# Kernel tuning notes

Hardware: AMD Instinct MI355X
Metric: run time of the kernel (lower is better)

## Reference

```python
import jax, jax.numpy as jnp
import numpy as np

D1 = 512
D2 = 1024  # = 2*D1 (concat of x1,y1 along channels)
B, S = 4, 2048


def _self_attn(x, Wq, bq, Wk, bk, Wv, bv):
    # Linear layers use torch convention: out = x @ W.T + b
    q = jnp.einsum('bsd,ed->bse', x, Wq) + bq
    k = jnp.einsum('bsd,ed->bse', x, Wk) + bk
    v = jnp.einsum('bsd,ed->bse', x, Wv) + bv
    # NOTE: original module has no 1/sqrt(d) scaling — keep it faithful.
    scores = jnp.einsum('bqe,bke->bqk', q, k)  # [B,S,S]
    attn = jax.nn.softmax(scores, axis=-1)
    return jnp.einsum('bqk,bke->bqe', attn, v)


def setup_inputs() -> dict:
    key = jax.random.key(0)
    ks = jax.random.split(key, 18)
    s1 = 1.0 / np.sqrt(D1)
    s2 = 1.0 / np.sqrt(D2)
    return {
        'x': jax.random.normal(ks[0], (B, S, D1), jnp.float32),
        'y': jax.random.normal(ks[1], (B, S, D1), jnp.float32),
        'sa1_Wq': jax.random.normal(ks[2], (D1, D1), jnp.float32) * s1,
        'sa1_bq': jnp.zeros((D1,), jnp.float32),
        'sa1_Wk': jax.random.normal(ks[3], (D1, D1), jnp.float32) * s1,
        'sa1_bk': jnp.zeros((D1,), jnp.float32),
        'sa1_Wv': jax.random.normal(ks[4], (D1, D1), jnp.float32) * s1,
        'sa1_bv': jnp.zeros((D1,), jnp.float32),
        'sa2_Wq': jax.random.normal(ks[5], (D2, D2), jnp.float32) * s2,
        'sa2_bq': jnp.zeros((D2,), jnp.float32),
        'sa2_Wk': jax.random.normal(ks[6], (D2, D2), jnp.float32) * s2,
        'sa2_bk': jnp.zeros((D2,), jnp.float32),
        'sa2_Wv': jax.random.normal(ks[7], (D2, D2), jnp.float32) * s2,
        'sa2_bv': jnp.zeros((D2,), jnp.float32),
        'weight1': jnp.ones((1,), jnp.float32),
        'weight2': jnp.ones((1,), jnp.float32),
    }


def reference(x, y, sa1_Wq, sa1_bq, sa1_Wk, sa1_bk, sa1_Wv, sa1_bv,
              sa2_Wq, sa2_bq, sa2_Wk, sa2_bk, sa2_Wv, sa2_bv,
              weight1, weight2):
    x1 = _self_attn(x, sa1_Wq, sa1_bq, sa1_Wk, sa1_bk, sa1_Wv, sa1_bv)
    x1 = x1 + y * weight2
    y1 = _self_attn(y, sa1_Wq, sa1_bq, sa1_Wk, sa1_bk, sa1_Wv, sa1_bv)
    y1 = y1 + x * weight1
    temp = jnp.concatenate((x1, y1), axis=2)  # [B,S,2*D1]
    return _self_attn(temp, sa2_Wq, sa2_bq, sa2_Wk, sa2_bk, sa2_Wv, sa2_bv)
```

## Files before the change

### kernel.cpp

```cpp
#include <hip/hip_runtime.h>
#include <hip/hip_bf16.h>
#include <cstdint>
#include <cstddef>


typedef __bf16 bf16;
typedef __attribute__((ext_vector_type(8))) __bf16 bf16x8;
typedef __attribute__((ext_vector_type(4))) __bf16 bf16x4;
typedef __attribute__((ext_vector_type(4))) float f32x4;

__device__ __forceinline__ void gld16(const bf16* g, bf16* s) {
    __builtin_amdgcn_global_load_lds(
        (const __attribute__((address_space(1))) void*)g,
        (__attribute__((address_space(3))) void*)s, 16, 0, 0);
}

#define WAIT_VM8   __builtin_amdgcn_s_waitcnt(8 | (7 << 4) | (0xF << 8))
#define WAIT_VM0   __builtin_amdgcn_s_waitcnt(0 | (7 << 4) | (0xF << 8))
#define WAIT_LGKM0 __builtin_amdgcn_s_waitcnt(0xF | (7 << 4) | (0 << 8) | (3 << 14))

__device__ __forceinline__ int swz(int row, int g) {
    return row * 64 + ((g ^ (row & 7)) << 3);
}

__global__ __launch_bounds__(256) void gemm_split(
    const bf16* __restrict__ A, long lda, long psA, long bsA,
    const bf16* __restrict__ B, long ldb, long psB, long bsB,
    void* __restrict__ C, long ldc, long psC, long bsC, int mode,
    const float* __restrict__ bias,
    const float* __restrict__ resid, long ldr, long bsR,
    const float* __restrict__ scale,
    int K, int split, int nx, int ny)
{
    __shared__ __align__(16) bf16 As[2][128 * 64];
    __shared__ __align__(16) bf16 Bs[2][128 * 64];

    const int t    = threadIdx.x;
    const int wave = t >> 6;
    const int lane = t & 63;
    const int wr   = wave >> 1;
    const int wc   = wave & 1;
    const int r16  = lane & 15;
    const int quad = lane >> 4;

    const int g    = blockIdx.x;
    const int xcd  = g & 7;
    const int tk   = g >> 3;
    const int nst8 = gridDim.x >> 7;
    const int st   = xcd * nst8 + (tk >> 4);
    const int p    = tk & 15;
    const int snx  = nx >> 2, sny = ny >> 2;
    const int spz  = snx * sny;
    const int zz   = st / spz;
    const int rS   = st - zz * spz;
    const int sy   = rS / snx;
    const int sx   = rS - sy * snx;
    const int yb   = sy * 4 + (p >> 2);
    const int xb   = sx * 4 + (p & 3);
    const long z   = zz;

    const long row0 = (long)yb * 128;
    const long col0 = (long)xb * 128;

    const int srow = (lane >> 3);
    const int scol = ((lane & 7) ^ srow) * 8;

    const int ktiles = K >> 6;
    const int T = split * ktiles;

    const bf16* Az = A + z * bsA;
    const bf16* Bz = B + z * bsB;

    auto prefetch = [&](int ti, int buf) {
        const int ph = ti / ktiles;
        const int kt = (ti - ph * ktiles) << 6;
        const bf16* Ab = Az + (ph == 1 ? psA : 0);
        const bf16* Bb = Bz + (ph == 2 ? psB : 0);
#pragma unroll
        for (int p2 = 0; p2 < 4; ++p2) {
            const int chunk = wave * 32 + p2 * 8;
            gld16(Ab + (row0 + chunk + srow) * lda + kt + scol, &As[buf][chunk * 64]);
            gld16(Bb + (col0 + chunk + srow) * ldb + kt + scol, &Bs[buf][chunk * 64]);
        }
    };

    f32x4 acc[4][4];
#pragma unroll
    for (int r = 0; r < 4; ++r)
#pragma unroll
        for (int c = 0; c < 4; ++c)
            acc[r][c] = (f32x4){0.f, 0.f, 0.f, 0.f};

    prefetch(0, 0);
    prefetch(1, 1);
    for (int ti = 0; ti < T; ++ti) {
        const int cur = ti & 1;
        if (ti + 1 < T) WAIT_VM8; else WAIT_VM0;
        __builtin_amdgcn_s_barrier();
        bf16x8 af[2][4], bg[2][4];
#pragma unroll
        for (int kk = 0; kk < 2; ++kk) {
            const int g0 = (kk << 2) + quad;
#pragma unroll
            for (int r = 0; r < 4; ++r)
                af[kk][r] = *reinterpret_cast<const bf16x8*>(&As[cur][swz(wr * 64 + r * 16 + r16, g0)]);
#pragma unroll
            for (int c = 0; c < 4; ++c)
                bg[kk][c] = *reinterpret_cast<const bf16x8*>(&Bs[cur][swz(wc * 64 + c * 16 + r16, g0)]);
        }
        WAIT_LGKM0;
        __builtin_amdgcn_s_barrier();
        if (ti + 2 < T) prefetch(ti + 2, cur);
#pragma unroll
        for (int kk = 0; kk < 2; ++kk)
#pragma unroll
            for (int r = 0; r < 4; ++r)
#pragma unroll
                for (int c = 0; c < 4; ++c)
                    acc[r][c] = __builtin_amdgcn_mfma_f32_16x16x32_bf16(af[kk][r], bg[kk][c], acc[r][c], 0, 0, 0);
    }

    const float scv = resid ? *scale : 0.f;

#pragma unroll
    for (int r = 0; r < 4; ++r) {
#pragma unroll
        for (int c = 0; c < 4; ++c) {
            long gcol = col0 + wc * 64 + c * 16 + r16;
            float bv = bias ? bias[gcol] : 0.f;
#pragma unroll
            for (int i = 0; i < 4; ++i) {
                long grow = row0 + wr * 64 + r * 16 + quad * 4 + i;
                float val = acc[r][c][i] + bv;
                if (mode == 0) {
                    if (resid) val += resid[z * bsR + grow * ldr + gcol] * scv;
                    ((float*)C)[z * bsC + grow * ldc + gcol] = val;
                } else if (mode == 1) {
                    if (resid) val += resid[z * bsR + grow * ldr + gcol] * scv;
                    bf16* Cb = (bf16*)C + z * bsC;
                    bf16 h = (bf16)val;
                    Cb[grow * ldc + gcol] = h;
                    Cb[psC + grow * ldc + gcol] = (bf16)(val - (float)h);
                } else {
                    long b = grow >> 11, s = grow & 2047;
                    bf16* Cb = (bf16*)C + b * bsC;
                    bf16 h = (bf16)val;
                    Cb[gcol * ldc + s] = h;
                    Cb[psC + gcol * ldc + s] = (bf16)(val - (float)h);
                }
            }
        }
    }
}

__global__ __launch_bounds__(512) void gemm256_scores(
    const bf16* __restrict__ A, long lda, long psA, long bsA,
    const bf16* __restrict__ B, long ldb, long psB, long bsB,
    float* __restrict__ C, long ldc, long bsC, int K)
{
    __shared__ __align__(16) bf16 As[2][256 * 64];
    __shared__ __align__(16) bf16 Bs[2][256 * 64];

    const int t    = threadIdx.x;
    const int wave = t >> 6;
    const int lane = t & 63;
    const int wm   = wave >> 2;
    const int wn   = wave & 3;
    const int r16  = lane & 15;
    const int quad = lane >> 4;

    const int g   = blockIdx.x;
    const int idx = (g & 7) * 32 + (g >> 3);
    const int z   = idx >> 6;
    const int t6  = idx & 63;
    const int ty  = t6 >> 3;
    const int tx  = t6 & 7;
    const long row0 = (long)ty * 256;
    const long col0 = (long)tx * 256;

    const int srow = lane >> 3;
    const int scol = ((lane & 7) ^ srow) * 8;

    const int ktiles = K >> 6;
    const int T = 3 * ktiles;

    const bf16* Az = A + (long)z * bsA;
    const bf16* Bz = B + (long)z * bsB;

    auto prefetch = [&](int ti, int buf) {
        const int ph = ti / ktiles;
        const int kt = (ti - ph * ktiles) << 6;
        const bf16* Ab = Az + (ph == 1 ? psA : 0);
        const bf16* Bb = Bz + (ph == 2 ? psB : 0);
#pragma unroll
        for (int p2 = 0; p2 < 4; ++p2) {
            const int chunk = wave * 32 + p2 * 8;
            gld16(Ab + (row0 + chunk + srow) * lda + kt + scol, &As[buf][chunk * 64]);
            gld16(Bb + (col0 + chunk + srow) * ldb + kt + scol, &Bs[buf][chunk * 64]);
        }
    };

    f32x4 acc[8][4];
#pragma unroll
    for (int r = 0; r < 8; ++r)
#pragma unroll
        for (int c = 0; c < 4; ++c)
            acc[r][c] = (f32x4){0.f, 0.f, 0.f, 0.f};

    prefetch(0, 0);
    prefetch(1, 1);
    for (int ti = 0; ti < T; ++ti) {
        const int cur = ti & 1;
        if (ti + 1 < T) WAIT_VM8; else WAIT_VM0;
        __builtin_amdgcn_s_barrier();

        bf16x8 afA[4][2], afB[4][2], bg[2][2][2];
#pragma unroll
        for (int kk = 0; kk < 2; ++kk) {
            const int g0 = (kk << 2) + quad;
#pragma unroll
            for (int r = 0; r < 4; ++r)
                afA[r][kk] = *reinterpret_cast<const bf16x8*>(
                    &As[cur][swz(wm * 128 + r * 16 + r16, g0)]);
        }
#pragma unroll
        for (int kk = 0; kk < 2; ++kk) {
            const int g0 = (kk << 2) + quad;
#pragma unroll
            for (int c = 0; c < 2; ++c)
                bg[0][c][kk] = *reinterpret_cast<const bf16x8*>(
                    &Bs[cur][swz(wn * 64 + c * 16 + r16, g0)]);
        }
#pragma unroll
        for (int kk = 0; kk < 2; ++kk) {
            const int g0 = (kk << 2) + quad;
#pragma unroll
            for (int c = 0; c < 2; ++c)
                bg[1][c][kk] = *reinterpret_cast<const bf16x8*>(
                    &Bs[cur][swz(wn * 64 + (2 + c) * 16 + r16, g0)]);
        }
#pragma unroll
        for (int kk = 0; kk < 2; ++kk) {
            const int g0 = (kk << 2) + quad;
#pragma unroll
            for (int r = 0; r < 4; ++r)
                afB[r][kk] = *reinterpret_cast<const bf16x8*>(
                    &As[cur][swz(wm * 128 + (4 + r) * 16 + r16, g0)]);
        }

        __builtin_amdgcn_s_setprio(1);
#pragma unroll
        for (int kk = 0; kk < 2; ++kk)
#pragma unroll
            for (int r = 0; r < 4; ++r)
#pragma unroll
                for (int c = 0; c < 2; ++c)
                    acc[r][c] = __builtin_amdgcn_mfma_f32_16x16x32_bf16(
                        afA[r][kk], bg[0][c][kk], acc[r][c], 0, 0, 0);
#pragma unroll
        for (int kk = 0; kk < 2; ++kk)
#pragma unroll
            for (int r = 0; r < 4; ++r)
#pragma unroll
                for (int c = 0; c < 2; ++c)
                    acc[r][2 + c] = __builtin_amdgcn_mfma_f32_16x16x32_bf16(
                        afA[r][kk], bg[1][c][kk], acc[r][2 + c], 0, 0, 0);
        __builtin_amdgcn_s_setprio(0);

        __builtin_amdgcn_sched_barrier(0);
        WAIT_LGKM0;
        __builtin_amdgcn_s_barrier();
        if (ti + 2 < T) prefetch(ti + 2, cur);

        __builtin_amdgcn_s_setprio(1);
#pragma unroll
        for (int kk = 0; kk < 2; ++kk)
#pragma unroll
            for (int r = 0; r < 4; ++r)
#pragma unroll
                for (int c = 0; c < 2; ++c)
                    acc[4 + r][c] = __builtin_amdgcn_mfma_f32_16x16x32_bf16(
                        afB[r][kk], bg[0][c][kk], acc[4 + r][c], 0, 0, 0);
#pragma unroll
        for (int kk = 0; kk < 2; ++kk)
#pragma unroll
            for (int r = 0; r < 4; ++r)
#pragma unroll
                for (int c = 0; c < 2; ++c)
                    acc[4 + r][2 + c] = __builtin_amdgcn_mfma_f32_16x16x32_bf16(
                        afB[r][kk], bg[1][c][kk], acc[4 + r][2 + c], 0, 0, 0);
        __builtin_amdgcn_s_setprio(0);
    }

#pragma unroll
    for (int r = 0; r < 8; ++r) {
#pragma unroll
        for (int c = 0; c < 4; ++c) {
            const long gcol = col0 + wn * 64 + c * 16 + r16;
#pragma unroll
            for (int i = 0; i < 4; ++i) {
                const long grow = row0 + wm * 128 + r * 16 + quad * 4 + i;
                C[(long)z * bsC + grow * ldc + gcol] = acc[r][c][i];
            }
        }
    }
}

__global__ __launch_bounds__(256) void softmax_planes(float* __restrict__ S)
{
    __shared__ float redm[4], reds[4];
    float* srow = S + (long)blockIdx.x * 2048;
    const int t = threadIdx.x;
    const int lane = t & 63;
    const int wave = t >> 6;

    f32x4 v0 = *reinterpret_cast<const f32x4*>(srow + t * 4);
    f32x4 v1 = *reinterpret_cast<const f32x4*>(srow + 1024 + t * 4);

    float m = v0[0];
#pragma unroll
    for (int i = 1; i < 4; ++i) m = fmaxf(m, v0[i]);
#pragma unroll
    for (int i = 0; i < 4; ++i) m = fmaxf(m, v1[i]);
#pragma unroll
    for (int off = 32; off > 0; off >>= 1) m = fmaxf(m, __shfl_xor(m, off));
    if (lane == 0) redm[wave] = m;
    __syncthreads();
    m = fmaxf(fmaxf(redm[0], redm[1]), fmaxf(redm[2], redm[3]));

    float s = 0.f;
#pragma unroll
    for (int i = 0; i < 4; ++i) { v0[i] = __expf(v0[i] - m); s += v0[i]; }
#pragma unroll
    for (int i = 0; i < 4; ++i) { v1[i] = __expf(v1[i] - m); s += v1[i]; }
#pragma unroll
    for (int off = 32; off > 0; off >>= 1) s += __shfl_xor(s, off);
    if (lane == 0) reds[wave] = s;
    __syncthreads();
    s = reds[0] + reds[1] + reds[2] + reds[3];
    float inv = 1.f / s;

    bf16x4 h0, h1, l0, l1;
#pragma unroll
    for (int i = 0; i < 4; ++i) {
        float a = v0[i] * inv, b = v1[i] * inv;
        h0[i] = (bf16)a; l0[i] = (bf16)(a - (float)h0[i]);
        h1[i] = (bf16)b; l1[i] = (bf16)(b - (float)h1[i]);
    }
    bf16* ph = (bf16*)srow;
    *reinterpret_cast<bf16x4*>(ph + t * 4) = h0;
    *reinterpret_cast<bf16x4*>(ph + 1024 + t * 4) = h1;
    *reinterpret_cast<bf16x4*>(ph + 2048 + t * 4) = l0;
    *reinterpret_cast<bf16x4*>(ph + 3072 + t * 4) = l1;
}

__global__ __launch_bounds__(256) void split_f32(
    const float* __restrict__ in, bf16* __restrict__ hi, long n)
{
    long i = ((long)blockIdx.x * 256 + threadIdx.x) * 4;
    f32x4 v = *reinterpret_cast<const f32x4*>(in + i);
    bf16x4 h, l;
#pragma unroll
    for (int j = 0; j < 4; ++j) {
        h[j] = (bf16)v[j];
        l[j] = (bf16)(v[j] - (float)h[j]);
    }
    *reinterpret_cast<bf16x4*>(hi + i) = h;
    *reinterpret_cast<bf16x4*>(hi + n + i) = l;
}

extern "C" void kernel_launch(void* const* d_in, const int* in_sizes, int n_in,
                              void* d_out, int out_size, void* d_ws, size_t ws_size,
                              hipStream_t stream)
{
    const float* x   = (const float*)d_in[0];
    const float* y   = (const float*)d_in[1];
    const float* Wq1 = (const float*)d_in[2];
    const float* bq1 = (const float*)d_in[3];
    const float* Wk1 = (const float*)d_in[4];
    const float* bk1 = (const float*)d_in[5];
    const float* Wv1 = (const float*)d_in[6];
    const float* bv1 = (const float*)d_in[7];
    const float* Wq2 = (const float*)d_in[8];
    const float* bq2 = (const float*)d_in[9];
    const float* Wk2 = (const float*)d_in[10];
    const float* bk2 = (const float*)d_in[11];
    const float* Wv2 = (const float*)d_in[12];
    const float* bv2 = (const float*)d_in[13];
    const float* w1  = (const float*)d_in[14];
    const float* w2  = (const float*)d_in[15];
    float* out = (float*)d_out;

    const size_t MB = 1ull << 20;
    char* ws = (char*)d_ws;
    const long S = 2048, M4 = 8192, E1 = 512, E2 = 1024;
    const long W1ps = E1 * E1, W2ps = E2 * E2;

    const int cfg = (ws_size >= 207 * MB) ? 2 : 0;

    bf16 *Wq1p, *Wk1p, *Wv1p, *Wq2p, *Wk2p, *Wv2p, *temp, *qb, *kb, *vt;
    float* Sc;
    bf16* xp = (bf16*)d_out;
    bf16* yp = xp + 2 * M4 * E1;
    if (cfg == 2) {
        Wq1p = (bf16*)(ws + 0 * MB);  Wk1p = (bf16*)(ws + 1 * MB);  Wv1p = (bf16*)(ws + 2 * MB);
        Wq2p = (bf16*)(ws + 3 * MB);  Wk2p = (bf16*)(ws + 7 * MB);  Wv2p = (bf16*)(ws + 11 * MB);
        temp = (bf16*)(ws + 15 * MB);
        qb   = (bf16*)(ws + 47 * MB);
        kb   = (bf16*)(ws + 79 * MB);
        vt   = (bf16*)(ws + 111 * MB);
        Sc   = (float*)(ws + 143 * MB);
    } else {
        Wq1p = (bf16*)(ws + 0 * MB);  Wk1p = (bf16*)(ws + 1 * MB);  Wv1p = (bf16*)(ws + 2 * MB);
        temp = (bf16*)(ws + 3 * MB);
        qb   = (bf16*)(ws + 35 * MB);
        kb   = (bf16*)(ws + 43 * MB);
        vt   = (bf16*)(ws + 51 * MB);
        Sc   = (float*)(ws + 59 * MB);
        Wq2p = (bf16*)d_out;
        Wk2p = Wq2p + 2 * W2ps;
        Wv2p = Wk2p + 2 * W2ps;
    }

    auto gemm = [&](const bf16* A, long lda, long psA, long bsA,
                    const bf16* B, long ldb, long psB, long bsB,
                    void* C, long ldc, long psC, long bsC, int mode,
                    const float* bias, const float* resid, long ldr, long bsR,
                    const float* scale, int M, int N, int K, int split, int gz) {
        int nx = N / 128, ny = M / 128;
        dim3 g((unsigned)(nx * ny * gz));
        gemm_split<<<g, dim3(256), 0, stream>>>(
            A, lda, psA, bsA, B, ldb, psB, bsB, C, ldc, psC, bsC, mode,
            bias, resid, ldr, bsR, scale, K, split, nx, ny);
    };
    auto scores256 = [&](const bf16* A, long lda, long psA, long bsA,
                         const bf16* B, long ldb, long psB, long bsB,
                         float* C, int K) {
        gemm256_scores<<<dim3(256), dim3(512), 0, stream>>>(
            A, lda, psA, bsA, B, ldb, psB, bsB, C, S, S * S, K);
    };
    auto conv = [&](const float* in, bf16* planes, long n) {
        split_f32<<<dim3((unsigned)(n / 1024)), dim3(256), 0, stream>>>(in, planes, n);
    };

    conv(x, xp, M4 * E1);
    conv(y, yp, M4 * E1);
    conv(Wq1, Wq1p, W1ps); conv(Wk1, Wk1p, W1ps); conv(Wv1, Wv1p, W1ps);
    if (cfg == 2) { conv(Wq2, Wq2p, W2ps); conv(Wk2, Wk2p, W2ps); conv(Wv2, Wv2p, W2ps); }

    auto stage1 = [&](const bf16* sp, const float* resid, const float* scale, long colOff) {
        if (cfg == 2) {
            gemm(sp, E1, M4 * E1, 0, Wq1p, E1, W1ps, 0, qb, E1, M4 * E1, 0, 1,
                 bq1, nullptr, 0, 0, nullptr, 8192, 512, 512, 3, 1);
            gemm(sp, E1, M4 * E1, 0, Wk1p, E1, W1ps, 0, kb, E1, M4 * E1, 0, 1,
                 bk1, nullptr, 0, 0, nullptr, 8192, 512, 512, 3, 1);
            gemm(sp, E1, M4 * E1, 0, Wv1p, E1, W1ps, 0, vt, S, E1 * S, 2 * E1 * S, 2,
                 bv1, nullptr, 0, 0, nullptr, 8192, 512, 512, 3, 1);
            scores256(qb, E1, M4 * E1, S * E1, kb, E1, M4 * E1, S * E1, Sc, 512);
            softmax_planes<<<dim3(8192), dim3(256), 0, stream>>>(Sc);
            gemm((const bf16*)Sc, 4096, 2048, S * 4096, vt, S, E1 * S, 2 * E1 * S,
                 temp + colOff, 1024, M4 * 1024, S * 1024, 1,
                 nullptr, resid, E1, S * E1, scale, 2048, 512, 2048, 3, 4);
        } else {
            for (int b = 0; b < 4; ++b) {
                const bf16* sb = sp + (long)b * S * E1;
                gemm(sb, E1, M4 * E1, 0, Wq1p, E1, W1ps, 0, qb, E1, S * E1, 0, 1,
                     bq1, nullptr, 0, 0, nullptr, 2048, 512, 512, 3, 1);
                gemm(sb, E1, M4 * E1, 0, Wk1p, E1, W1ps, 0, kb, E1, S * E1, 0, 1,
                     bk1, nullptr, 0, 0, nullptr, 2048, 512, 512, 3, 1);
                gemm(sb, E1, M4 * E1, 0, Wv1p, E1, W1ps, 0, vt, S, E1 * S, 0, 2,
                     bv1, nullptr, 0, 0, nullptr, 2048, 512, 512, 3, 1);
                gemm(qb, E1, S * E1, 0, kb, E1, S * E1, 0, Sc, S, 0, 0, 0,
                     nullptr, nullptr, 0, 0, nullptr, 2048, 2048, 512, 3, 1);
                softmax_planes<<<dim3(2048), dim3(256), 0, stream>>>(Sc);
                gemm((const bf16*)Sc, 4096, 2048, 0, vt, S, E1 * S, 0,
                     temp + colOff + (long)b * S * 1024, 1024, M4 * 1024, 0, 1,
                     nullptr, resid + (long)b * S * E1, E1, 0, scale, 2048, 512, 2048, 3, 1);
            }
        }
    };

    stage1(xp, y, w2, 0);
    stage1(yp, x, w1, 512);

    if (cfg == 0) { conv(Wq2, Wq2p, W2ps); conv(Wk2, Wk2p, W2ps); conv(Wv2, Wv2p, W2ps); }

    if (cfg == 2) {
        gemm(temp, E2, M4 * E2, 0, Wq2p, E2, W2ps, 0, qb, E2, M4 * E2, 0, 1,
             bq2, nullptr, 0, 0, nullptr, 8192, 1024, 1024, 3, 1);
        gemm(temp, E2, M4 * E2, 0, Wk2p, E2, W2ps, 0, kb, E2, M4 * E2, 0, 1,
             bk2, nullptr, 0, 0, nullptr, 8192, 1024, 1024, 3, 1);
        gemm(temp, E2, M4 * E2, 0, Wv2p, E2, W2ps, 0, vt, S, E2 * S, 2 * E2 * S, 2,
             bv2, nullptr, 0, 0, nullptr, 8192, 1024, 1024, 1, 1);
        scores256(qb, E2, M4 * E2, S * E2, kb, E2, M4 * E2, S * E2, Sc, 1024);
        softmax_planes<<<dim3(8192), dim3(256), 0, stream>>>(Sc);
        gemm((const bf16*)Sc, 4096, 2048, S * 4096, vt, S, E2 * S, 2 * E2 * S,
             out, E2, 0, S * E2, 0, nullptr, nullptr, 0, 0, nullptr,
             2048, 1024, 2048, 1, 4);
    } else {
        for (int b = 0; b < 4; ++b) {
            const bf16* tb = temp + (long)b * S * E2;
            gemm(tb, E2, M4 * E2, 0, Wq2p, E2, W2ps, 0, qb, E2, S * E2, 0, 1,
                 bq2, nullptr, 0, 0, nullptr, 2048, 1024, 1024, 3, 1);
            gemm(tb, E2, M4 * E2, 0, Wk2p, E2, W2ps, 0, kb, E2, S * E2, 0, 1,
                 bk2, nullptr, 0, 0, nullptr, 2048, 1024, 1024, 3, 1);
            gemm(tb, E2, M4 * E2, 0, Wv2p, E2, W2ps, 0, vt, S, E2 * S, 0, 2,
                 bv2, nullptr, 0, 0, nullptr, 2048, 1024, 1024, 1, 1);
            gemm(qb, E2, S * E2, 0, kb, E2, S * E2, 0, Sc, S, 0, 0, 0,
                 nullptr, nullptr, 0, 0, nullptr, 2048, 2048, 1024, 3, 1);
            softmax_planes<<<dim3(2048), dim3(256), 0, stream>>>(Sc);
            gemm((const bf16*)Sc, 4096, 2048, 0, vt, S, E2 * S, 0,
                 out + (long)b * S * E2, E2, 0, 0, 0, nullptr, nullptr, 0, 0, nullptr,
                 2048, 1024, 2048, 1, 1);
        }
    }

    (void)in_sizes; (void)n_in; (void)out_size;
}
```

Measured before the change: 986.5 us.

## Fuse Q/K projections and batch x/y stage-1 projections into single GEMMs

For the large-workspace path, Wq and Wk are concatenated into one weight matrix so Q and K come from a single GEMM, with a split bias selected per column. The x and y inputs are packed contiguously so the stage-1 projections for both run as one GEMM with M=16384 instead of separate launches. This cuts kernel launches and rereads of the A operand, and gives each GEMM a larger grid. In exchange the weight and activation buffers need reorganized plane layouts, and the epilogue does a per-column branch to pick the bias.

```diff
diff --git a/kernel.cpp b/kernel.cpp
--- a/kernel.cpp
+++ b/kernel.cpp
@@ -27,7 +27,7 @@
     const bf16* __restrict__ A, long lda, long psA, long bsA,
     const bf16* __restrict__ B, long ldb, long psB, long bsB,
     void* __restrict__ C, long ldc, long psC, long bsC, int mode,
-    const float* __restrict__ bias,
+    const float* __restrict__ bias, const float* __restrict__ bias2, int nsplit,
     const float* __restrict__ resid, long ldr, long bsR,
     const float* __restrict__ scale,
     int K, int split, int nx, int ny)
@@ -127,7 +127,8 @@
 #pragma unroll
         for (int c = 0; c < 4; ++c) {
             long gcol = col0 + wc * 64 + c * 16 + r16;
-            float bv = bias ? bias[gcol] : 0.f;
+            float bv = 0.f;
+            if (bias) bv = (gcol < nsplit) ? bias[gcol] : bias2[gcol - nsplit];
 #pragma unroll
             for (int i = 0; i < 4; ++i) {
                 long grow = row0 + wr * 64 + r * 16 + quad * 4 + i;
@@ -354,8 +355,8 @@
     *reinterpret_cast<bf16x4*>(ph + 3072 + t * 4) = l1;
 }
 
-__global__ __launch_bounds__(256) void split_f32(
-    const float* __restrict__ in, bf16* __restrict__ hi, long n)
+__global__ __launch_bounds__(256) void split2_f32(
+    const float* __restrict__ in, bf16* __restrict__ hi, bf16* __restrict__ lo)
 {
     long i = ((long)blockIdx.x * 256 + threadIdx.x) * 4;
     f32x4 v = *reinterpret_cast<const f32x4*>(in + i);
@@ -366,7 +367,7 @@
         l[j] = (bf16)(v[j] - (float)h[j]);
     }
     *reinterpret_cast<bf16x4*>(hi + i) = h;
-    *reinterpret_cast<bf16x4*>(hi + n + i) = l;
+    *reinterpret_cast<bf16x4*>(lo + i) = l;
 }
 
 extern "C" void kernel_launch(void* const* d_in, const int* in_sizes, int n_in,
@@ -398,40 +399,17 @@
 
     const int cfg = (ws_size >= 207 * MB) ? 2 : 0;
 
-    bf16 *Wq1p, *Wk1p, *Wv1p, *Wq2p, *Wk2p, *Wv2p, *temp, *qb, *kb, *vt;
-    float* Sc;
-    bf16* xp = (bf16*)d_out;
-    bf16* yp = xp + 2 * M4 * E1;
-    if (cfg == 2) {
-        Wq1p = (bf16*)(ws + 0 * MB);  Wk1p = (bf16*)(ws + 1 * MB);  Wv1p = (bf16*)(ws + 2 * MB);
-        Wq2p = (bf16*)(ws + 3 * MB);  Wk2p = (bf16*)(ws + 7 * MB);  Wv2p = (bf16*)(ws + 11 * MB);
-        temp = (bf16*)(ws + 15 * MB);
-        qb   = (bf16*)(ws + 47 * MB);
-        kb   = (bf16*)(ws + 79 * MB);
-        vt   = (bf16*)(ws + 111 * MB);
-        Sc   = (float*)(ws + 143 * MB);
-    } else {
-        Wq1p = (bf16*)(ws + 0 * MB);  Wk1p = (bf16*)(ws + 1 * MB);  Wv1p = (bf16*)(ws + 2 * MB);
-        temp = (bf16*)(ws + 3 * MB);
-        qb   = (bf16*)(ws + 35 * MB);
-        kb   = (bf16*)(ws + 43 * MB);
-        vt   = (bf16*)(ws + 51 * MB);
-        Sc   = (float*)(ws + 59 * MB);
-        Wq2p = (bf16*)d_out;
-        Wk2p = Wq2p + 2 * W2ps;
-        Wv2p = Wk2p + 2 * W2ps;
-    }
-
     auto gemm = [&](const bf16* A, long lda, long psA, long bsA,
                     const bf16* B, long ldb, long psB, long bsB,
                     void* C, long ldc, long psC, long bsC, int mode,
-                    const float* bias, const float* resid, long ldr, long bsR,
+                    const float* bias, const float* bias2, int nsplit,
+                    const float* resid, long ldr, long bsR,
                     const float* scale, int M, int N, int K, int split, int gz) {
         int nx = N / 128, ny = M / 128;
         dim3 g((unsigned)(nx * ny * gz));
         gemm_split<<<g, dim3(256), 0, stream>>>(
             A, lda, psA, bsA, B, ldb, psB, bsB, C, ldc, psC, bsC, mode,
-            bias, resid, ldr, bsR, scale, K, split, nx, ny);
+            bias, bias2, nsplit, resid, ldr, bsR, scale, K, split, nx, ny);
     };
     auto scores256 = [&](const bf16* A, long lda, long psA, long bsA,
                          const bf16* B, long ldb, long psB, long bsB,
@@ -439,79 +417,131 @@
         gemm256_scores<<<dim3(256), dim3(512), 0, stream>>>(
             A, lda, psA, bsA, B, ldb, psB, bsB, C, S, S * S, K);
     };
-    auto conv = [&](const float* in, bf16* planes, long n) {
-        split_f32<<<dim3((unsigned)(n / 1024)), dim3(256), 0, stream>>>(in, planes, n);
+    auto conv2 = [&](const float* in, bf16* hi, bf16* lo, long n) {
+        split2_f32<<<dim3((unsigned)(n / 1024)), dim3(256), 0, stream>>>(in, hi, lo);
     };
 
-    conv(x, xp, M4 * E1);
-    conv(y, yp, M4 * E1);
-    conv(Wq1, Wq1p, W1ps); conv(Wk1, Wk1p, W1ps); conv(Wv1, Wv1p, W1ps);
-    if (cfg == 2) { conv(Wq2, Wq2p, W2ps); conv(Wk2, Wk2p, W2ps); conv(Wv2, Wv2p, W2ps); }
-
-    auto stage1 = [&](const bf16* sp, const float* resid, const float* scale, long colOff) {
-        if (cfg == 2) {
-            gemm(sp, E1, M4 * E1, 0, Wq1p, E1, W1ps, 0, qb, E1, M4 * E1, 0, 1,
-                 bq1, nullptr, 0, 0, nullptr, 8192, 512, 512, 3, 1);
-            gemm(sp, E1, M4 * E1, 0, Wk1p, E1, W1ps, 0, kb, E1, M4 * E1, 0, 1,
-                 bk1, nullptr, 0, 0, nullptr, 8192, 512, 512, 3, 1);
-            gemm(sp, E1, M4 * E1, 0, Wv1p, E1, W1ps, 0, vt, S, E1 * S, 2 * E1 * S, 2,
-                 bv1, nullptr, 0, 0, nullptr, 8192, 512, 512, 3, 1);
-            scores256(qb, E1, M4 * E1, S * E1, kb, E1, M4 * E1, S * E1, Sc, 512);
-            softmax_planes<<<dim3(8192), dim3(256), 0, stream>>>(Sc);
-            gemm((const bf16*)Sc, 4096, 2048, S * 4096, vt, S, E1 * S, 2 * E1 * S,
-                 temp + colOff, 1024, M4 * 1024, S * 1024, 1,
-                 nullptr, resid, E1, S * E1, scale, 2048, 512, 2048, 3, 4);
-        } else {
+    if (cfg == 2) {
+        bf16* xyp   = (bf16*)d_out;
+        bf16* Wqk1p = (bf16*)(ws + 0 * MB);
+        bf16* Wv1p  = (bf16*)(ws + 2 * MB);
+        bf16* Wqk2p = (bf16*)(ws + 3 * MB);
+        bf16* Wv2p  = (bf16*)(ws + 11 * MB);
+        bf16* temp  = (bf16*)(ws + 15 * MB);
+        bf16* qk    = (bf16*)(ws + 47 * MB);
+        bf16* vt    = (bf16*)(ws + 111 * MB);
+        float* Sc   = (float*)(ws + 143 * MB);
+
+        const long PXY = 16384L * 512;
+        const long PW1 = 1024L * 512;
+        const long PW2 = 2048L * 1024;
+        const long PQ1 = 16384L * 1024;
+        const long PQ2 = 8192L * 2048;
+        const long PT  = 8192L * 1024;
+        const long BV1 = 2 * E1 * S;
+        const long BV2 = 2 * E2 * S;
+
+        conv2(x, xyp, xyp + PXY, M4 * E1);
+        conv2(y, xyp + M4 * E1, xyp + PXY + M4 * E1, M4 * E1);
+        conv2(Wq1, Wqk1p, Wqk1p + PW1, W1ps);
+        conv2(Wk1, Wqk1p + W1ps, Wqk1p + PW1 + W1ps, W1ps);
+        conv2(Wv1, Wv1p, Wv1p + W1ps, W1ps);
+        conv2(Wq2, Wqk2p, Wqk2p + PW2, W2ps);
+        conv2(Wk2, Wqk2p + W2ps, Wqk2p + PW2 + W2ps, W2ps);
+        conv2(Wv2, Wv2p, Wv2p + W2ps, W2ps);
+
+        gemm(xyp, E1, PXY, 0, Wqk1p, E1, PW1, 0,
+             qk, 1024, PQ1, 0, 1, bq1, bk1, 512,
+             nullptr, 0, 0, nullptr, 16384, 1024, 512, 3, 1);
+        gemm(xyp, E1, PXY, 0, Wv1p, E1, W1ps, 0,
+             vt, S, E1 * S, BV1, 2, bv1, nullptr, 512,
+             nullptr, 0, 0, nullptr, 16384, 512, 512, 3, 1);
+
+        scores256(qk, 1024, PQ1, S * 1024, qk + 512, 1024, PQ1, S * 1024, Sc, 512);
+        softmax_planes<<<dim3(8192), dim3(256), 0, stream>>>(Sc);
+        gemm((const bf16*)Sc, 4096, 2048, S * 4096, vt, S, E1 * S, BV1,
+             temp, 1024, PT, S * 1024, 1, nullptr, nullptr, 512,
+             y, E1, S * E1, w2, 2048, 512, 2048, 3, 4);
+
+        scores256(qk + M4 * 1024, 1024, PQ1, S * 1024,
+                  qk + M4 * 1024 + 512, 1024, PQ1, S * 1024, Sc, 512);
+        softmax_planes<<<dim3(8192), dim3(256), 0, stream>>>(Sc);
+        gemm((const bf16*)Sc, 4096, 2048, S * 4096, vt + 4 * BV1, S, E1 * S, BV1,
+             temp + 512, 1024, PT, S * 1024, 1, nullptr, nullptr, 512,
+             x, E1, S * E1, w1, 2048, 512, 2048, 3, 4);
+
+        gemm(temp, E2, PT, 0, Wqk2p, E2, PW2, 0,
+             qk, 2048, PQ2, 0, 1, bq2, bk2, 1024,
+             nullptr, 0, 0, nullptr, 8192, 2048, 1024, 3, 1);
+        gemm(temp, E2, PT, 0, Wv2p, E2, W2ps, 0,
+             vt, S, E2 * S, BV2, 2, bv2, nullptr, 1024,
+             nullptr, 0, 0, nullptr, 8192, 1024, 1024, 1, 1);
+        scores256(qk, 2048, PQ2, S * 2048, qk + 1024, 2048, PQ2, S * 2048, Sc, 1024);
+        softmax_planes<<<dim3(8192), dim3(256), 0, stream>>>(Sc);
+        gemm((const bf16*)Sc, 4096, 2048, S * 4096, vt, S, E2 * S, BV2,
+             out, E2, 0, S * E2, 0, nullptr, nullptr, 1024,
+             nullptr, 0, 0, nullptr, 2048, 1024, 2048, 1, 4);
+    } else {
+        bf16* xp = (bf16*)d_out;
+        bf16* yp = xp + 2 * M4 * E1;
+        bf16* Wq1p = (bf16*)(ws + 0 * MB);
+        bf16* Wk1p = (bf16*)(ws + 1 * MB);
+        bf16* Wv1p = (bf16*)(ws + 2 * MB);
+        bf16* temp = (bf16*)(ws + 3 * MB);
+        bf16* qb   = (bf16*)(ws + 35 * MB);
+        bf16* kb   = (bf16*)(ws + 43 * MB);
+        bf16* vt   = (bf16*)(ws + 51 * MB);
+        float* Sc  = (float*)(ws + 59 * MB);
+        bf16* Wq2p = (bf16*)d_out;
+        bf16* Wk2p = Wq2p + 2 * W2ps;
+        bf16* Wv2p = Wk2p + 2 * W2ps;
+
+        conv2(x, xp, xp + M4 * E1, M4 * E1);
+        conv2(y, yp, yp + M4 * E1, M4 * E1);
+        conv2(Wq1, Wq1p, Wq1p + W1ps, W1ps);
+        conv2(Wk1, Wk1p, Wk1p + W1ps, W1ps);
+        conv2(Wv1, Wv1p, Wv1p + W1ps, W1ps);
+
+        auto stage1 = [&](const bf16* sp, const float* resid, const float* scale, long colOff) {
             for (int b = 0; b < 4; ++b) {
                 const bf16* sb = sp + (long)b * S * E1;
                 gemm(sb, E1, M4 * E1, 0, Wq1p, E1, W1ps, 0, qb, E1, S * E1, 0, 1,
-                     bq1, nullptr, 0, 0, nullptr, 2048, 512, 512, 3, 1);
+                     bq1, nullptr, 512, nullptr, 0, 0, nullptr, 2048, 512, 512, 3, 1);
                 gemm(sb, E1, M4 * E1, 0, Wk1p, E1, W1ps, 0, kb, E1, S * E1, 0, 1,
-                     bk1, nullptr, 0, 0, nullptr, 2048, 512, 512, 3, 1);
+                     bk1, nullptr, 512, nullptr, 0, 0, nullptr, 2048, 512, 512, 3, 1);
                 gemm(sb, E1, M4 * E1, 0, Wv1p, E1, W1ps, 0, vt, S, E1 * S, 0, 2,
-                     bv1, nullptr, 0, 0, nullptr, 2048, 512, 512, 3, 1);
+                     bv1, nullptr, 512, nullptr, 0, 0, nullptr, 2048, 512, 512, 3, 1);
                 gemm(qb, E1, S * E1, 0, kb, E1, S * E1, 0, Sc, S, 0, 0, 0,
-                     nullptr, nullptr, 0, 0, nullptr, 2048, 2048, 512, 3, 1);
+                     nullptr, nullptr, 2048, nullptr, 0, 0, nullptr, 2048, 2048, 512, 3, 1);
                 softmax_planes<<<dim3(2048), dim3(256), 0, stream>>>(Sc);
                 gemm((const bf16*)Sc, 4096, 2048, 0, vt, S, E1 * S, 0,
                      temp + colOff + (long)b * S * 1024, 1024, M4 * 1024, 0, 1,
-                     nullptr, resid + (long)b * S * E1, E1, 0, scale, 2048, 512, 2048, 3, 1);
+                     nullptr, nullptr, 512, resid + (long)b * S * E1, E1, 0, scale,
+                     2048, 512, 2048, 3, 1);
             }
-        }
-    };
-
-    stage1(xp, y, w2, 0);
-    stage1(yp, x, w1, 512);
-
-    if (cfg == 0) { conv(Wq2, Wq2p, W2ps); conv(Wk2, Wk2p, W2ps); conv(Wv2, Wv2p, W2ps); }
-
-    if (cfg == 2) {
-        gemm(temp, E2, M4 * E2, 0, Wq2p, E2, W2ps, 0, qb, E2, M4 * E2, 0, 1,
-             bq2, nullptr, 0, 0, nullptr, 8192, 1024, 1024, 3, 1);
-        gemm(temp, E2, M4 * E2, 0, Wk2p, E2, W2ps, 0, kb, E2, M4 * E2, 0, 1,
-             bk2, nullptr, 0, 0, nullptr, 8192, 1024, 1024, 3, 1);
-        gemm(temp, E2, M4 * E2, 0, Wv2p, E2, W2ps, 0, vt, S, E2 * S, 2 * E2 * S, 2,
-             bv2, nullptr, 0, 0, nullptr, 8192, 1024, 1024, 1, 1);
-        scores256(qb, E2, M4 * E2, S * E2, kb, E2, M4 * E2, S * E2, Sc, 1024);
-        softmax_planes<<<dim3(8192), dim3(256), 0, stream>>>(Sc);
-        gemm((const bf16*)Sc, 4096, 2048, S * 4096, vt, S, E2 * S, 2 * E2 * S,
-             out, E2, 0, S * E2, 0, nullptr, nullptr, 0, 0, nullptr,
-             2048, 1024, 2048, 1, 4);
-    } else {
+        };
+
+        stage1(xp, y, w2, 0);
+        stage1(yp, x, w1, 512);
+
+        conv2(Wq2, Wq2p, Wq2p + W2ps, W2ps);
+        conv2(Wk2, Wk2p, Wk2p + W2ps, W2ps);
+        conv2(Wv2, Wv2p, Wv2p + W2ps, W2ps);
+
         for (int b = 0; b < 4; ++b) {
             const bf16* tb = temp + (long)b * S * E2;
             gemm(tb, E2, M4 * E2, 0, Wq2p, E2, W2ps, 0, qb, E2, S * E2, 0, 1,
-                 bq2, nullptr, 0, 0, nullptr, 2048, 1024, 1024, 3, 1);
+                 bq2, nullptr, 1024, nullptr, 0, 0, nullptr, 2048, 1024, 1024, 3, 1);
             gemm(tb, E2, M4 * E2, 0, Wk2p, E2, W2ps, 0, kb, E2, S * E2, 0, 1,
-                 bk2, nullptr, 0, 0, nullptr, 2048, 1024, 1024, 3, 1);
+                 bk2, nullptr, 1024, nullptr, 0, 0, nullptr, 2048, 1024, 1024, 3, 1);
             gemm(tb, E2, M4 * E2, 0, Wv2p, E2, W2ps, 0, vt, S, E2 * S, 0, 2,
-                 bv2, nullptr, 0, 0, nullptr, 2048, 1024, 1024, 1, 1);
+                 bv2, nullptr, 1024, nullptr, 0, 0, nullptr, 2048, 1024, 1024, 1, 1);
             gemm(qb, E2, S * E2, 0, kb, E2, S * E2, 0, Sc, S, 0, 0, 0,
-                 nullptr, nullptr, 0, 0, nullptr, 2048, 2048, 1024, 3, 1);
+                 nullptr, nullptr, 2048, nullptr, 0, 0, nullptr, 2048, 2048, 1024, 3, 1);
             softmax_planes<<<dim3(2048), dim3(256), 0, stream>>>(Sc);
             gemm((const bf16*)Sc, 4096, 2048, 0, vt, S, E2 * S, 0,
-                 out + (long)b * S * E2, E2, 0, 0, 0, nullptr, nullptr, 0, 0, nullptr,
-                 2048, 1024, 2048, 1, 1);
+                 out + (long)b * S * E2, E2, 0, 0, 0, nullptr, nullptr, 1024,
+                 nullptr, 0, 0, nullptr, 2048, 1024, 2048, 1, 1);
         }
     }
 
```

After: 920.1 us. -6.7%, faster.
